# Optimization experiments

Hardware: AMD Instinct MI355X
Metric: run time of the kernel (lower is better)

## Reference

```python
import jax, jax.numpy as jnp
import numpy as np

H = 4
N = 50000
D_IN = 128
D_MODEL = 256
NCLASS = 40
B_S = 1
BH = B_S * H
LN_EPS = 1e-5


def sparse_perm_1D(indices, values, feats, n, bh):
    """Batched sparse (bh,n,n) @ dense (bh,n,d): gather -> scale -> segment-sum scatter."""
    gathered = feats[indices[0], indices[2]]              # (nnz, d)
    contrib = values[:, None] * gathered                   # (nnz, d)
    seg = indices[0] * n + indices[1]                      # (nnz,)
    out = jax.ops.segment_sum(contrib, seg, num_segments=bh * n)
    return out.reshape(bh, n, -1)


def layer_norm(x, gamma, beta):
    mu = jnp.mean(x, axis=-1, keepdims=True)
    var = jnp.var(x, axis=-1, keepdims=True)
    return (x - mu) * jax.lax.rsqrt(var + LN_EPS) * gamma + beta


def setup_inputs() -> dict:
    key = jax.random.key(0)
    k1, k2, k3, k4, k5, k6, k7 = jax.random.split(key, 7)
    # per-(batch*head) permutation sigma: nonzero at (b, i, sigma_b(i))
    perm_keys = jax.random.split(k1, BH)
    sigma = jax.vmap(lambda k: jax.random.permutation(k, N))(perm_keys)  # (BH, N)
    b_idx = jnp.repeat(jnp.arange(BH), N)
    row_idx = jnp.tile(jnp.arange(N), BH)
    col_idx = sigma.reshape(-1)
    perm_indices = jnp.stack([b_idx, row_idx, col_idx], axis=0).astype(jnp.int32)  # (3, BH*N)
    perm_values = jax.random.uniform(k2, (BH * N,), dtype=jnp.float32)
    features = jax.random.normal(k3, (B_S, N, D_IN), dtype=jnp.float32)
    appd = jax.random.normal(k4, (B_S, N, D_IN), dtype=jnp.float32)
    # parameters
    w_scale_in = 1.0 / np.sqrt(2 * D_IN)
    W_in = jax.random.uniform(k5, (2 * D_IN, D_MODEL), dtype=jnp.float32, minval=-w_scale_in, maxval=w_scale_in)
    b_in = jnp.zeros((D_MODEL,), dtype=jnp.float32)
    ln_gamma = jnp.ones((D_MODEL * H,), dtype=jnp.float32)
    ln_beta = jnp.zeros((D_MODEL * H,), dtype=jnp.float32)
    w_scale_h = 1.0 / np.sqrt(D_MODEL * H)
    W_head = jax.random.uniform(k6, (D_MODEL * H, NCLASS), dtype=jnp.float32, minval=-w_scale_h, maxval=w_scale_h)
    b_head = jax.random.uniform(k7, (NCLASS,), dtype=jnp.float32, minval=-w_scale_h, maxval=w_scale_h)
    return {"perm_indices": perm_indices, "perm_values": perm_values,
            "features": features, "appd": appd,
            "W_in": W_in, "b_in": b_in,
            "ln_gamma": ln_gamma, "ln_beta": ln_beta,
            "W_head": W_head, "b_head": b_head}


def reference(perm_indices, perm_values, features, appd, W_in, b_in, ln_gamma, ln_beta, W_head, b_head):
    # concat auxiliary features, replicate per head: (B_S,N,2*D_IN) -> (BH,N,2*D_IN)
    feat = jnp.concatenate([features, appd], axis=-1)
    feat = jnp.broadcast_to(feat[:, None], (B_S, H, N, 2 * D_IN)).reshape(BH, N, 2 * D_IN)
    # permute rows: perm @ feat
    x = sparse_perm_1D(perm_indices, perm_values, feat, N, BH)
    # ff_in + relu (dropout is identity at eval)
    x = jax.nn.relu(x @ W_in + b_in)                       # (BH, N, D_MODEL)
    # nlayers == nblocks == 0: compress/uncompress loops are empty
    # inverse permutation: perm^T @ x (swap row/col indices)
    idx_t = jnp.stack([perm_indices[0], perm_indices[2], perm_indices[1]], axis=0)
    y = sparse_perm_1D(idx_t, perm_values, x, N, BH)       # (BH, N, D_MODEL)
    # (B_S,H,N,D) -> (B_S,N,H*D)
    y = y.reshape(B_S, H, N, D_MODEL).transpose(0, 2, 1, 3).reshape(B_S, N, H * D_MODEL)
    y = layer_norm(y, ln_gamma, ln_beta)
    return y @ W_head + b_head                             # (B_S, N, NCLASS)
```

## Files before the change

### kernel.cpp

```cpp
#include <hip/hip_runtime.h>
#include <hip/hip_bf16.h>

#define NROW 50000
#define DIN 128
#define DM 256
#define HH 4
#define NC 40
#define BHN 200000
#define NBLK 1563

typedef float f32x4 __attribute__((ext_vector_type(4)));
typedef short bf16x8 __attribute__((ext_vector_type(8)));

__device__ __forceinline__ unsigned int pk2(float lo, float hi) {
    __hip_bfloat162 h = __float22bfloat162_rn(make_float2(lo, hi));
    return *(unsigned int*)&h;
}

__global__ __launch_bounds__(256) void k_prep(const int* __restrict__ pi,
                                              const float* __restrict__ pv,
                                              const float* __restrict__ Win,
                                              const float* __restrict__ Wh,
                                              const float* __restrict__ gamma,
                                              const float* __restrict__ beta,
                                              const float* __restrict__ bh,
                                              float* __restrict__ vcol,
                                              unsigned short* __restrict__ Wpk,
                                              unsigned short* __restrict__ Wgpk,
                                              float* __restrict__ bias2,
                                              float* __restrict__ wsum) {
    const int bid = blockIdx.x, tid = threadIdx.x;
    if (bid < 196) {
        int k4 = (bid * 256 + tid) * 4;
        if (k4 < BHN) {
            int4   c4 = *(const int4*)&pi[2 * BHN + k4];
            float4 v4 = *(const float4*)&pv[k4];
            int b = (k4 >= 150000) ? 3 : (k4 >= 100000) ? 2 : (k4 >= 50000) ? 1 : 0;
            float* vb = vcol + b * NROW;
            vb[c4.x] = v4.x; vb[c4.y] = v4.y; vb[c4.z] = v4.z; vb[c4.w] = v4.w;
        }
    } else if (bid < 212) {
        int base = (bid - 196) * 512;
        #pragma unroll
        for (int qq = 0; qq < 2; ++qq) {
            int s = base + qq * 256 + tid;
            int ln = s & 63;
            int t  = (s >> 6) & 15;
            int kc = s >> 10;
            int n  = t * 16 + (ln & 15);
            int kb = kc * 32 + ((ln >> 4) << 3);
            union { unsigned int ui[4]; uint4 v4; } u;
            #pragma unroll
            for (int jj = 0; jj < 4; ++jj)
                u.ui[jj] = pk2(Win[(kb + 2 * jj) * DM + n], Win[(kb + 2 * jj + 1) * DM + n]);
            *(uint4*)&Wpk[s * 8] = u.v4;
        }
    } else if (bid < 224) {
        int base = (bid - 212) * 512;
        #pragma unroll
        for (int qq = 0; qq < 2; ++qq) {
            int s = base + qq * 256 + tid;
            int ln = s & 63;
            int u6 = s >> 6;
            int t  = u6 % 3;
            int v6 = u6 / 3;
            int kc = v6 & 7;
            int h  = v6 >> 3;
            int c  = t * 16 + (ln & 15);
            int dbase = h * 256 + kc * 32 + ((ln >> 4) << 2);
            union { unsigned int ui[4]; uint4 v4; } u;
            if (c < NC) {
                #pragma unroll
                for (int jj = 0; jj < 4; ++jj) {
                    int dA = dbase + ((jj >> 1) << 4) + ((jj & 1) << 1);
                    u.ui[jj] = pk2(gamma[dA] * Wh[dA * NC + c],
                                   gamma[dA + 1] * Wh[(dA + 1) * NC + c]);
                }
            } else {
                u.v4 = make_uint4(0u, 0u, 0u, 0u);
            }
            *(uint4*)&Wgpk[s * 8] = u.v4;
        }
    } else {
        __shared__ float redb[256], redw[256];
        int c = bid - 224;
        float sb = 0.f, sw = 0.f;
        #pragma unroll
        for (int q = 0; q < 4; ++q) {
            int d = tid + 256 * q;
            float w = Wh[d * NC + c];
            sb = fmaf(beta[d], w, sb);
            sw = fmaf(gamma[d], w, sw);
        }
        redb[tid] = sb; redw[tid] = sw;
        __syncthreads();
        for (int st = 128; st > 0; st >>= 1) {
            if (tid < st) { redb[tid] += redb[tid + st]; redw[tid] += redw[tid + st]; }
            __syncthreads();
        }
        if (tid == 0) { bias2[c] = bh[c] + redb[0]; wsum[c] = redw[0]; }
    }
}

#define Y_PASS(VH, ACC, S, SS, HALF) { \
    _Pragma("unroll") \
    for (int tt = 0; tt < 8; ++tt) { \
        float4 b4 = *(const float4*)&bshm[((HALF) * 8 + tt) * 16 + quad * 4]; \
        float y0 = (VH) * fmaxf(fmaf((VH), ACC[tt][0], b4.x), 0.f); \
        float y1 = (VH) * fmaxf(fmaf((VH), ACC[tt][1], b4.y), 0.f); \
        float y2 = (VH) * fmaxf(fmaf((VH), ACC[tt][2], b4.z), 0.f); \
        float y3 = (VH) * fmaxf(fmaf((VH), ACC[tt][3], b4.w), 0.f); \
        S += (y0 + y1) + (y2 + y3); \
        SS = fmaf(y0, y0, SS); SS = fmaf(y1, y1, SS); \
        SS = fmaf(y2, y2, SS); SS = fmaf(y3, y3, SS); \
        ya[tt * 2]     = pk2(y0, y1); \
        ya[tt * 2 + 1] = pk2(y2, y3); \
    } }

#define HEAD_MFMA(ACCO) { \
    _Pragma("unroll") \
    for (int kcr = 0; kcr < 4; ++kcr) { \
        union { unsigned int ui[4]; bf16x8 v; } af; \
        af.ui[0] = ya[4 * kcr];     af.ui[1] = ya[4 * kcr + 1]; \
        af.ui[2] = ya[4 * kcr + 2]; af.ui[3] = ya[4 * kcr + 3]; \
        _Pragma("unroll") \
        for (int t3 = 0; t3 < 3; ++t3) \
            ACCO[t3] = __builtin_amdgcn_mfma_f32_16x16x32_bf16( \
                af.v, wg[kcr * 3 + t3], ACCO[t3], 0, 0, 0); \
    } }

#define AFR_PACK(AFR, AR) { \
    const float* rf = feats + (size_t)(AR) * DIN; \
    const float* ra = appd  + (size_t)(AR) * DIN; \
    _Pragma("unroll") \
    for (int kc = 0; kc < 8; ++kc) { \
        const float* src = (kc < 4) ? rf : ra; \
        const int ko = (kc & 3) * 32 + quad * 8; \
        float4 x0 = *(const float4*)(src + ko); \
        float4 x1 = *(const float4*)(src + ko + 4); \
        AFR[kc][0] = pk2(x0.x, x0.y); \
        AFR[kc][1] = pk2(x0.z, x0.w); \
        AFR[kc][2] = pk2(x1.x, x1.y); \
        AFR[kc][3] = pk2(x1.z, x1.w); \
    } }

__global__ __launch_bounds__(64, 2) void k_fused(
    const float* __restrict__ feats, const float* __restrict__ appd,
    const unsigned short* __restrict__ Wpk,
    const unsigned short* __restrict__ Wgpk,
    const float* __restrict__ vcol,
    const float* __restrict__ b_in,
    const float* __restrict__ bias2,
    const float* __restrict__ wsum,
    float* __restrict__ out)
{
    __shared__ __align__(16) float bshm[256];

    const int tid = threadIdx.x;
    const int ln = tid;
    const int quad = ln >> 4;
    const int lr = ln & 15;
    const int jw = blockIdx.x * 32;
    const int ar0 = min(jw + lr, NROW - 1);
    const int ar1 = min(jw + 16 + lr, NROW - 1);

    #pragma unroll
    for (int q = 0; q < 4; ++q) bshm[tid + 64 * q] = b_in[tid + 64 * q];
    __syncthreads();

    float vm0[HH], vm1[HH];
    #pragma unroll
    for (int h = 0; h < HH; ++h) {
        vm0[h] = vcol[h * NROW + ar0];
        vm1[h] = vcol[h * NROW + ar1];
    }

    const unsigned short* wpL = Wpk  + (size_t)ln * 8;
    const unsigned short* wgL = Wgpk + (size_t)ln * 8;

    const f32x4 zero4 = {0.f, 0.f, 0.f, 0.f};
    float s0 = 0.f, ss0 = 0.f, s1 = 0.f, ss1 = 0.f;
    f32x4 accO0[3], accO1[3];
    #pragma unroll
    for (int t = 0; t < 3; ++t) { accO0[t] = zero4; accO1[t] = zero4; }
    f32x4 accG0[8], accG1[8];
    unsigned int ya[16];

    #pragma unroll
    for (int half = 0; half < 2; ++half) {
        if (half == 1) asm volatile("" ::: "memory");

        unsigned int afr0[8][4], afr1[8][4];
        AFR_PACK(afr0, ar0)
        AFR_PACK(afr1, ar1)

        #pragma unroll
        for (int kc = 0; kc < 8; ++kc) {
            asm volatile("" ::: "memory");
            bf16x8 wf[8];
            #pragma unroll
            for (int th = 0; th < 8; ++th)
                wf[th] = *(const bf16x8*)&wpL[(size_t)(kc * 16 + half * 8 + th) * 512];
            union { unsigned int ui[4]; bf16x8 v; } a0, a1;
            a0.ui[0] = afr0[kc][0]; a0.ui[1] = afr0[kc][1];
            a0.ui[2] = afr0[kc][2]; a0.ui[3] = afr0[kc][3];
            a1.ui[0] = afr1[kc][0]; a1.ui[1] = afr1[kc][1];
            a1.ui[2] = afr1[kc][2]; a1.ui[3] = afr1[kc][3];
            #pragma unroll
            for (int th = 0; th < 8; ++th) {
                accG0[th] = __builtin_amdgcn_mfma_f32_16x16x32_bf16(
                    wf[th], a0.v, (kc == 0) ? zero4 : accG0[th], 0, 0, 0);
                accG1[th] = __builtin_amdgcn_mfma_f32_16x16x32_bf16(
                    wf[th], a1.v, (kc == 0) ? zero4 : accG1[th], 0, 0, 0);
            }
        }

        #pragma unroll
        for (int h = 0; h < HH; ++h) {
            asm volatile("" ::: "memory");
            bf16x8 wg[12];
            #pragma unroll
            for (int kcr = 0; kcr < 2; ++kcr)
                #pragma unroll
                for (int t3 = 0; t3 < 3; ++t3)
                    wg[kcr * 3 + t3] = *(const bf16x8*)
                        &wgL[(size_t)(((h * 8 + half * 4 + kcr) * 3 + t3)) * 512];
            Y_PASS(vm0[h], accG0, s0, ss0, half)
            #pragma unroll
            for (int kcr = 2; kcr < 4; ++kcr)
                #pragma unroll
                for (int t3 = 0; t3 < 3; ++t3)
                    wg[kcr * 3 + t3] = *(const bf16x8*)
                        &wgL[(size_t)(((h * 8 + half * 4 + kcr) * 3 + t3)) * 512];
            HEAD_MFMA(accO0)
            Y_PASS(vm1[h], accG1, s1, ss1, half)
            HEAD_MFMA(accO1)
        }
    }

    s0  += __shfl_xor(s0, 16);  s0  += __shfl_xor(s0, 32);
    ss0 += __shfl_xor(ss0, 16); ss0 += __shfl_xor(ss0, 32);
    s1  += __shfl_xor(s1, 16);  s1  += __shfl_xor(s1, 32);
    ss1 += __shfl_xor(ss1, 16); ss1 += __shfl_xor(ss1, 32);
    float mm0  = s0 * (1.f / 1024.f);
    float rs0  = rsqrtf(ss0 * (1.f / 1024.f) - mm0 * mm0 + 1e-5f);
    float nm0  = -mm0 * rs0;
    float mm1  = s1 * (1.f / 1024.f);
    float rs1  = rsqrtf(ss1 * (1.f / 1024.f) - mm1 * mm1 + 1e-5f);
    float nm1  = -mm1 * rs1;

    float rs_r0[4], nm_r0[4], rs_r1[4], nm_r1[4];
    #pragma unroll
    for (int rg = 0; rg < 4; ++rg) {
        int rloc = quad * 4 + rg;
        rs_r0[rg] = __shfl(rs0, rloc);
        nm_r0[rg] = __shfl(nm0, rloc);
        rs_r1[rg] = __shfl(rs1, rloc);
        nm_r1[rg] = __shfl(nm1, rloc);
    }
    #pragma unroll
    for (int t = 0; t < 3; ++t) {
        int c = t * 16 + lr;
        if (c < NC) {
            float w2 = wsum[c], b2 = bias2[c];
            #pragma unroll
            for (int rg = 0; rg < 4; ++rg) {
                int row0 = jw + quad * 4 + rg;
                int row1 = row0 + 16;
                if (row0 < NROW)
                    out[(size_t)row0 * NC + c] = fmaf(rs_r0[rg], accO0[t][rg], fmaf(nm_r0[rg], w2, b2));
                if (row1 < NROW)
                    out[(size_t)row1 * NC + c] = fmaf(rs_r1[rg], accO1[t][rg], fmaf(nm_r1[rg], w2, b2));
            }
        }
    }
}

extern "C" void kernel_launch(void* const* d_in, const int* in_sizes, int n_in,
                              void* d_out, int out_size, void* d_ws, size_t ws_size,
                              hipStream_t stream) {
    const int*   pi    = (const int*)d_in[0];
    const float* pv    = (const float*)d_in[1];
    const float* feats = (const float*)d_in[2];
    const float* appd  = (const float*)d_in[3];
    const float* Win   = (const float*)d_in[4];
    const float* b_in  = (const float*)d_in[5];
    const float* gamma = (const float*)d_in[6];
    const float* beta  = (const float*)d_in[7];
    const float* Wh    = (const float*)d_in[8];
    const float* bh    = (const float*)d_in[9];
    float* out = (float*)d_out;

    char* w = (char*)d_ws;
    float*          vcolW  = (float*)w;
    unsigned short* WpkW   = (unsigned short*)(w + 800000);
    unsigned short* WgpkW  = (unsigned short*)(w + 931072);
    float*          bias2W = (float*)(w + 1029376);
    float*          wsumW  = (float*)(w + 1029536);

    k_prep<<<264, 256, 0, stream>>>(pi, pv, Win, Wh, gamma, beta, bh,
                                    vcolW, WpkW, WgpkW, bias2W, wsumW);
    k_fused<<<NBLK, 64, 0, stream>>>(feats, appd, WpkW, WgpkW, vcolW, b_in,
                                     bias2W, wsumW, out);
}
```

Before: 141.2 us.

## Share packed weights across four waves via LDS using direct global-to-LDS loads

The fused kernel now runs 256-thread blocks of four waves, each covering 32 rows, instead of one wave per block. The packed W_in and head-weight fragments are staged once per block into a 64KB shared buffer with global_load_lds and read from LDS, where before each wave fetched them from global memory on its own. This cuts redundant weight traffic and L2 pressure. The cost is added block-wide barriers and heavy LDS use, which may limit occupancy and make waves wait on each other.

```diff
diff --git a/kernel.cpp b/kernel.cpp
--- a/kernel.cpp
+++ b/kernel.cpp
@@ -7,7 +7,7 @@
 #define HH 4
 #define NC 40
 #define BHN 200000
-#define NBLK 1563
+#define NBLK 391
 
 typedef float f32x4 __attribute__((ext_vector_type(4)));
 typedef short bf16x8 __attribute__((ext_vector_type(8)));
@@ -15,6 +15,13 @@
 __device__ __forceinline__ unsigned int pk2(float lo, float hi) {
     __hip_bfloat162 h = __float22bfloat162_rn(make_float2(lo, hi));
     return *(unsigned int*)&h;
+}
+
+__device__ __forceinline__ void gl_lds16(const unsigned short* g, unsigned short* l) {
+    __builtin_amdgcn_global_load_lds(
+        (const __attribute__((address_space(1))) unsigned int*)(g),
+        (__attribute__((address_space(3))) unsigned int*)(l),
+        16, 0, 0);
 }
 
 __global__ __launch_bounds__(256) void k_prep(const int* __restrict__ pi,
@@ -105,7 +112,7 @@
 #define Y_PASS(VH, ACC, S, SS, HALF) { \
     _Pragma("unroll") \
     for (int tt = 0; tt < 8; ++tt) { \
-        float4 b4 = *(const float4*)&bshm[((HALF) * 8 + tt) * 16 + quad * 4]; \
+        float4 b4 = *(const float4*)&bshm[(HALF) * 128 + tt * 16 + quad * 4]; \
         float y0 = (VH) * fmaxf(fmaf((VH), ACC[tt][0], b4.x), 0.f); \
         float y1 = (VH) * fmaxf(fmaf((VH), ACC[tt][1], b4.y), 0.f); \
         float y2 = (VH) * fmaxf(fmaf((VH), ACC[tt][2], b4.z), 0.f); \
@@ -129,12 +136,10 @@
                 af.v, wg[kcr * 3 + t3], ACCO[t3], 0, 0, 0); \
     } }
 
-#define AFR_PACK(AFR, AR) { \
-    const float* rf = feats + (size_t)(AR) * DIN; \
-    const float* ra = appd  + (size_t)(AR) * DIN; \
+#define AFR_PACK(AFR, F, A) { \
     _Pragma("unroll") \
     for (int kc = 0; kc < 8; ++kc) { \
-        const float* src = (kc < 4) ? rf : ra; \
+        const float* src = (kc < 4) ? (F) : (A); \
         const int ko = (kc & 3) * 32 + quad * 8; \
         float4 x0 = *(const float4*)(src + ko); \
         float4 x1 = *(const float4*)(src + ko + 4); \
@@ -144,7 +149,7 @@
         AFR[kc][3] = pk2(x1.z, x1.w); \
     } }
 
-__global__ __launch_bounds__(64, 2) void k_fused(
+__global__ __launch_bounds__(256, 2) void k_fused(
     const float* __restrict__ feats, const float* __restrict__ appd,
     const unsigned short* __restrict__ Wpk,
     const unsigned short* __restrict__ Wgpk,
@@ -154,19 +159,24 @@
     const float* __restrict__ wsum,
     float* __restrict__ out)
 {
+    __shared__ __align__(16) unsigned short wsh[32768];
     __shared__ __align__(16) float bshm[256];
 
     const int tid = threadIdx.x;
-    const int ln = tid;
+    const int wv = tid >> 6;
+    const int ln = tid & 63;
     const int quad = ln >> 4;
     const int lr = ln & 15;
-    const int jw = blockIdx.x * 32;
+    const int jw = blockIdx.x * 128 + wv * 32;
     const int ar0 = min(jw + lr, NROW - 1);
     const int ar1 = min(jw + 16 + lr, NROW - 1);
 
-    #pragma unroll
-    for (int q = 0; q < 4; ++q) bshm[tid + 64 * q] = b_in[tid + 64 * q];
-    __syncthreads();
+    bshm[tid] = b_in[tid];
+
+    const float* f0 = feats + (size_t)ar0 * DIN;
+    const float* a0 = appd  + (size_t)ar0 * DIN;
+    const float* f1 = feats + (size_t)ar1 * DIN;
+    const float* a1 = appd  + (size_t)ar1 * DIN;
 
     float vm0[HH], vm1[HH];
     #pragma unroll
@@ -175,24 +185,31 @@
         vm1[h] = vcol[h * NROW + ar1];
     }
 
-    const unsigned short* wpL = Wpk  + (size_t)ln * 8;
-    const unsigned short* wgL = Wgpk + (size_t)ln * 8;
-
     const f32x4 zero4 = {0.f, 0.f, 0.f, 0.f};
     float s0 = 0.f, ss0 = 0.f, s1 = 0.f, ss1 = 0.f;
     f32x4 accO0[3], accO1[3];
     #pragma unroll
     for (int t = 0; t < 3; ++t) { accO0[t] = zero4; accO1[t] = zero4; }
-    f32x4 accG0[8], accG1[8];
-    unsigned int ya[16];
 
     #pragma unroll
     for (int half = 0; half < 2; ++half) {
         if (half == 1) asm volatile("" ::: "memory");
 
+        #pragma unroll
+        for (int q = 0; q < 16; ++q) {
+            int s = wv * 16 + q;
+            int kc = s >> 3, th = s & 7;
+            gl_lds16(Wpk + ((size_t)((kc * 16 + half * 8 + th) * 64 + ln)) * 8,
+                     &wsh[s * 512]);
+        }
         unsigned int afr0[8][4], afr1[8][4];
-        AFR_PACK(afr0, ar0)
-        AFR_PACK(afr1, ar1)
+        AFR_PACK(afr0, f0, a0)
+        AFR_PACK(afr1, f1, a1)
+        __syncthreads();
+
+        f32x4 accG0[8], accG1[8];
+        #pragma unroll
+        for (int t = 0; t < 8; ++t) { accG0[t] = zero4; accG1[t] = zero4; }
 
         #pragma unroll
         for (int kc = 0; kc < 8; ++kc) {
@@ -200,42 +217,45 @@
             bf16x8 wf[8];
             #pragma unroll
             for (int th = 0; th < 8; ++th)
-                wf[th] = *(const bf16x8*)&wpL[(size_t)(kc * 16 + half * 8 + th) * 512];
-            union { unsigned int ui[4]; bf16x8 v; } a0, a1;
-            a0.ui[0] = afr0[kc][0]; a0.ui[1] = afr0[kc][1];
-            a0.ui[2] = afr0[kc][2]; a0.ui[3] = afr0[kc][3];
-            a1.ui[0] = afr1[kc][0]; a1.ui[1] = afr1[kc][1];
-            a1.ui[2] = afr1[kc][2]; a1.ui[3] = afr1[kc][3];
+                wf[th] = *(const bf16x8*)&wsh[((kc * 8 + th) * 64 + ln) * 8];
+            union { unsigned int ui[4]; bf16x8 v; } av0, av1;
+            av0.ui[0] = afr0[kc][0]; av0.ui[1] = afr0[kc][1];
+            av0.ui[2] = afr0[kc][2]; av0.ui[3] = afr0[kc][3];
+            av1.ui[0] = afr1[kc][0]; av1.ui[1] = afr1[kc][1];
+            av1.ui[2] = afr1[kc][2]; av1.ui[3] = afr1[kc][3];
             #pragma unroll
             for (int th = 0; th < 8; ++th) {
-                accG0[th] = __builtin_amdgcn_mfma_f32_16x16x32_bf16(
-                    wf[th], a0.v, (kc == 0) ? zero4 : accG0[th], 0, 0, 0);
-                accG1[th] = __builtin_amdgcn_mfma_f32_16x16x32_bf16(
-                    wf[th], a1.v, (kc == 0) ? zero4 : accG1[th], 0, 0, 0);
+                accG0[th] = __builtin_amdgcn_mfma_f32_16x16x32_bf16(wf[th], av0.v, accG0[th], 0, 0, 0);
+                accG1[th] = __builtin_amdgcn_mfma_f32_16x16x32_bf16(wf[th], av1.v, accG1[th], 0, 0, 0);
             }
         }
+        __syncthreads();
+
+        #pragma unroll
+        for (int q = 0; q < 12; ++q) {
+            int kcr = q / 3, t3 = q % 3;
+            gl_lds16(Wgpk + ((size_t)(((wv * 8 + half * 4 + kcr) * 3 + t3) * 64 + ln)) * 8,
+                     &wsh[(wv * 12 + q) * 512]);
+        }
+        __syncthreads();
 
         #pragma unroll
         for (int h = 0; h < HH; ++h) {
             asm volatile("" ::: "memory");
             bf16x8 wg[12];
             #pragma unroll
-            for (int kcr = 0; kcr < 2; ++kcr)
+            for (int kcr = 0; kcr < 4; ++kcr)
                 #pragma unroll
                 for (int t3 = 0; t3 < 3; ++t3)
                     wg[kcr * 3 + t3] = *(const bf16x8*)
-                        &wgL[(size_t)(((h * 8 + half * 4 + kcr) * 3 + t3)) * 512];
+                        &wsh[((h * 12 + kcr * 3 + t3) * 64 + ln) * 8];
+            unsigned int ya[16];
             Y_PASS(vm0[h], accG0, s0, ss0, half)
-            #pragma unroll
-            for (int kcr = 2; kcr < 4; ++kcr)
-                #pragma unroll
-                for (int t3 = 0; t3 < 3; ++t3)
-                    wg[kcr * 3 + t3] = *(const bf16x8*)
-                        &wgL[(size_t)(((h * 8 + half * 4 + kcr) * 3 + t3)) * 512];
             HEAD_MFMA(accO0)
             Y_PASS(vm1[h], accG1, s1, ss1, half)
             HEAD_MFMA(accO1)
         }
+        __syncthreads();
     }
 
     s0  += __shfl_xor(s0, 16);  s0  += __shfl_xor(s0, 32);
@@ -300,6 +320,6 @@
 
     k_prep<<<264, 256, 0, stream>>>(pi, pv, Win, Wh, gamma, beta, bh,
                                     vcolW, WpkW, WgpkW, bias2W, wsumW);
-    k_fused<<<NBLK, 64, 0, stream>>>(feats, appd, WpkW, WgpkW, vcolW, b_in,
-                                     bias2W, wsumW, out);
-}
+    k_fused<<<NBLK, 256, 0, stream>>>(feats, appd, WpkW, WgpkW, vcolW, b_in,
+                                      bias2W, wsumW, out);
+}
```

Result: slower. 153.1 us (+8.5%).
